# Performance work log

Measured on AMD Instinct MI355X. Metric: run time of the kernel, lower is better.

## Reference

```python
import jax, jax.numpy as jnp
import numpy as np

LAM = 0.5
B, N, C = 512, 197, 384


def _mlp(x, w1, b1, w2, b2):
    # Linear -> exact GELU -> Linear (dropout is identity in eval)
    h = jax.nn.gelu(x @ w1 + b1, approximate=False)
    return h @ w2 + b2


def _ln(x, g, b, eps=1e-5):
    m = jnp.mean(x, axis=-1, keepdims=True)
    v = jnp.mean((x - m) ** 2, axis=-1, keepdims=True)
    return (x - m) * jax.lax.rsqrt(v + eps) * g + b


def _l2norm(x, eps=1e-12):
    n = jnp.sqrt(jnp.sum(x * x, axis=-1, keepdims=True))
    return x / jnp.maximum(n, eps)


def setup_inputs() -> dict:
    key = jax.random.key(0)
    ks = iter(jax.random.split(key, 40))
    s = 0.02

    def w(shape):
        return (jax.random.normal(next(ks), shape, jnp.float32) * s)

    inp = {
        'feat_query': jax.random.normal(next(ks), (B, N, C), jnp.float32),
        'feat_shot': jax.random.normal(next(ks), (B, N, C), jnp.float32),
        'feat_query_start': jax.random.normal(next(ks), (B, N, C), jnp.float32),
        'feat_shot_start': jax.random.normal(next(ks), (B, N, C), jnp.float32),
        # fc1: 384 -> 96 -> 384
        'fc1_w1': w((384, 96)), 'fc1_b1': jnp.zeros((96,)),
        'fc1_w2': w((96, 384)), 'fc1_b2': jnp.zeros((384,)),
        'ln1_g': jnp.ones((384,)), 'ln1_b': jnp.zeros((384,)),
        # fc3: 196 -> 128 -> 196
        'fc3_w1': w((196, 128)), 'fc3_b1': jnp.zeros((128,)),
        'fc3_w2': w((128, 196)), 'fc3_b2': jnp.zeros((196,)),
        'ln3_g': jnp.ones((196,)), 'ln3_b': jnp.zeros((196,)),
        # fc4: 384 -> 96 -> 384
        'fc4_w1': w((384, 96)), 'fc4_b1': jnp.zeros((96,)),
        'fc4_w2': w((96, 384)), 'fc4_b2': jnp.zeros((384,)),
        'ln4_g': jnp.ones((384,)), 'ln4_b': jnp.zeros((384,)),
        # fc2: 9604 -> 256 -> 1
        'fc2_w1': w((98 * 98, 256)), 'fc2_b1': jnp.zeros((256,)),
        'fc2_w2': w((256, 1)), 'fc2_b2': jnp.zeros((1,)),
        # cosine_sim.layer1: 384 -> 96 -> 384
        'cs_w1': w((384, 96)), 'cs_b1': jnp.zeros((96,)),
        'cs_w2': w((96, 384)), 'cs_b2': jnp.zeros((384,)),
    }
    return inp


def reference(feat_query, feat_shot, feat_query_start, feat_shot_start,
              fc1_w1, fc1_b1, fc1_w2, fc1_b2, ln1_g, ln1_b,
              fc3_w1, fc3_b1, fc3_w2, fc3_b2, ln3_g, ln3_b,
              fc4_w1, fc4_b1, fc4_w2, fc4_b2, ln4_g, ln4_b,
              fc2_w1, fc2_b1, fc2_w2, fc2_b2,
              cs_w1, cs_b1, cs_w2, cs_b2):
    def fc1_res(x):  # Mlp over mean token, added back (broadcast over seq)
        m = jnp.mean(x, axis=1, keepdims=True)  # [B,1,C]
        return _ln(_mlp(m, fc1_w1, fc1_b1, fc1_w2, fc1_b2) + x, ln1_g, ln1_b)

    fq = fc1_res(feat_query)
    fs = fc1_res(feat_shot)
    fqs = fc1_res(feat_query_start)
    fss = fc1_res(feat_shot_start)

    query_class = fq[:, 0:1, :]          # [B,1,384]
    query_image = fq[:, 1:, :]           # [B,196,384]
    query_image_start = fqs[:, 1:, :]
    support_class = fs[:, 0:1, :]
    support_image = fs[:, 1:, :]
    support_image_start = fss[:, 1:, :]

    def fc3_path(x):  # Mlp over token dim (196) + LN(196)
        xt = jnp.swapaxes(x, -1, -2)     # [B,384,196]
        xt = _ln(_mlp(xt, fc3_w1, fc3_b1, fc3_w2, fc3_b2), ln3_g, ln3_b)
        return jnp.swapaxes(xt, -1, -2)

    query_image_start = fc3_path(query_image_start)
    support_image_start = fc3_path(support_image_start)

    query_image = _ln(_mlp(query_image * query_image_start, fc4_w1, fc4_b1, fc4_w2, fc4_b2), ln4_g, ln4_b)
    support_image = _ln(_mlp(support_image * support_image_start, fc4_w1, fc4_b1, fc4_w2, fc4_b2), ln4_g, ln4_b)

    fq2 = query_image + LAM * query_class
    fs2 = support_image + LAM * support_class
    fq2 = _l2norm(fq2)
    fq2 = fq2 - jnp.mean(fq2, axis=2, keepdims=True)
    fs2 = _l2norm(fs2)
    fs2 = fs2 - jnp.mean(fs2, axis=2, keepdims=True)

    out = jnp.einsum('bqc,bsc->bqs', fq2, fs2)        # [B,196,196]
    b = out.shape[0]
    out = out.reshape(b, 98, 2, 98, 2).mean(axis=(2, 4))  # AvgPool2d(2,2)
    out = out.reshape(b, 98 * 98)
    out = (_mlp_fc2(out ** 2, fc2_w1, fc2_b1, fc2_w2, fc2_b2)).squeeze(-1)  # [B]

    # Cosine_Sim on class tokens
    qx = _mlp(query_class[:, 0, :], cs_w1, cs_b1, cs_w2, cs_b2)
    sy = _mlp(support_class[:, 0, :], cs_w1, cs_b1, cs_w2, cs_b2)
    eps = 1e-8
    cosine = jnp.sum(qx * sy, axis=-1) / (
        jnp.maximum(jnp.linalg.norm(qx, axis=-1), eps) * jnp.maximum(jnp.linalg.norm(sy, axis=-1), eps))

    return out, cosine, query_class, support_class


def _mlp_fc2(x, w1, b1, w2, b2):
    h = jax.nn.gelu(x @ w1 + b1, approximate=False)
    return h @ w2 + b2
```

## Files before the change

kernel.cpp:

```cpp
#include <hip/hip_runtime.h>
#include <math.h>

typedef unsigned short ushort_t;
typedef __attribute__((ext_vector_type(8))) short bf16x8;
typedef __attribute__((ext_vector_type(4))) float f32x4;

__device__ __forceinline__ float geluf(float x){
  return 0.5f*x*(1.0f+erff(x*0.70710678118654752440f));
}
__device__ __forceinline__ float bfu(unsigned int u){
  union { unsigned int i; float f; } v; v.i = (u & 0xffffu) << 16; return v.f;
}
__device__ __forceinline__ unsigned int f2b(float f){
  union { float f; unsigned int i; } v; v.f = f;
  unsigned int r = v.i + 0x7fffu + ((v.i >> 16) & 1u);
  return (r >> 16);
}


__global__ __launch_bounds__(384) void k_mean(
    const float* __restrict__ x0, const float* __restrict__ x1,
    const float* __restrict__ x2, const float* __restrict__ x3,
    float* __restrict__ meanb){
  __shared__ float4 red[4][96];
  int sb = blockIdx.x;
  int s = sb >> 9, b = sb & 511;
  const float* x = (s==0)?x0:(s==1)?x1:(s==2)?x2:x3;
  int tid = threadIdx.x;
  int c4 = tid % 96, g = tid / 96;
  const float* p = x + ((size_t)b*197)*384 + c4*4;
  float4 acc = {0.f,0.f,0.f,0.f};
  for (int t = g; t < 197; t += 4){
    float4 v = *reinterpret_cast<const float4*>(p + (size_t)t*384);
    acc.x += v.x; acc.y += v.y; acc.z += v.z; acc.w += v.w;
  }
  red[g][c4] = acc;
  __syncthreads();
  if (tid < 96){
    float4 a = red[0][tid], bb = red[1][tid], c = red[2][tid], d = red[3][tid];
    float4 o;
    o.x = (a.x+bb.x+c.x+d.x)*(1.0f/197.0f);
    o.y = (a.y+bb.y+c.y+d.y)*(1.0f/197.0f);
    o.z = (a.z+bb.z+c.z+d.z)*(1.0f/197.0f);
    o.w = (a.w+bb.w+c.w+d.w)*(1.0f/197.0f);
    *reinterpret_cast<float4*>(&meanb[(size_t)sb*384 + tid*4]) = o;
  }
}

__global__ __launch_bounds__(384) void k_fc1(
    const float* __restrict__ meanb, const float* __restrict__ w1,
    const float* __restrict__ b1, const float* __restrict__ w2,
    const float* __restrict__ b2, float* __restrict__ mlp1){
  __shared__ float ms[384];
  __shared__ float hs[96];
  int row = blockIdx.x, tid = threadIdx.x;
  ms[tid] = meanb[(size_t)row*384 + tid];
  __syncthreads();
  if (tid < 96){
    float a = b1[tid];
    for (int c=0;c<384;++c) a += ms[c]*w1[c*96+tid];
    hs[tid] = geluf(a);
  }
  __syncthreads();
  float a = b2[tid];
  for (int j=0;j<96;++j) a += hs[j]*w2[j*384+tid];
  mlp1[(size_t)row*384 + tid] = a;
}

__global__ __launch_bounds__(256) void k_stats(
    const float* __restrict__ x0, const float* __restrict__ x1,
    const float* __restrict__ x2, const float* __restrict__ x3,
    const float* __restrict__ mlp1, float* __restrict__ mu, float* __restrict__ rstd){
  int sb = blockIdx.x;
  int s = sb >> 9, b = sb & 511;
  const float* x = (s==0)?x0:(s==1)?x1:(s==2)?x2:x3;
  const float* mp = mlp1 + (size_t)sb*384;
  int tid = threadIdx.x, w = tid >> 6, lane = tid & 63;
  int g = lane >> 4, il = lane & 15;
  float4 mreg[6];
  #pragma unroll
  for (int it = 0; it < 6; ++it)
    mreg[it] = *reinterpret_cast<const float4*>(&mp[il*4 + 64*it]);
  for (int t0 = 0; t0 < 208; t0 += 16){
    int t = t0 + w*4 + g;
    if (t < 197){
      const float* xp = x + ((size_t)b*197 + t)*384 + il*4;
      float sum = 0.f, sq = 0.f;
      #pragma unroll
      for (int it = 0; it < 6; ++it){
        float4 v = *reinterpret_cast<const float4*>(xp + 64*it);
        float a0 = v.x + mreg[it].x, a1 = v.y + mreg[it].y;
        float a2 = v.z + mreg[it].z, a3 = v.w + mreg[it].w;
        sum += a0+a1+a2+a3;
        sq  += a0*a0+a1*a1+a2*a2+a3*a3;
      }
      #pragma unroll
      for (int o=1;o<16;o<<=1){ sum += __shfl_xor(sum,o); sq += __shfl_xor(sq,o); }
      if (il == 0){
        int row = sb*197 + t;
        float m = sum*(1.0f/384.0f);
        mu[row] = m;
        rstd[row] = rsqrtf(sq*(1.0f/384.0f) - m*m + 1e-5f);
      }
    }
  }
}

__global__ __launch_bounds__(384) void k_class(
    const float* __restrict__ x0, const float* __restrict__ x1,
    const float* __restrict__ mlp1, const float* __restrict__ mu,
    const float* __restrict__ rstd, const float* __restrict__ g1,
    const float* __restrict__ bb1, float* __restrict__ dout){
  int s = blockIdx.x >> 9, b = blockIdx.x & 511, c = threadIdx.x;
  const float* x = s ? x1 : x0;
  int srow = (s*512 + b)*197;
  float v = x[((size_t)b*197)*384 + c] + mlp1[((size_t)s*512+b)*384 + c];
  float y = (v - mu[srow])*rstd[srow]*g1[c] + bb1[c];
  dout[1024 + (size_t)s*196608 + (size_t)b*384 + c] = y;
}

__global__ __launch_bounds__(384) void k_cosine(
    const float* __restrict__ w1, const float* __restrict__ b1,
    const float* __restrict__ w2, const float* __restrict__ b2,
    float* __restrict__ dout){
  __shared__ float qrow[384], srw[384], hq[96], hs[96];
  __shared__ float rd0[384], rd1[384], rd2[384];
  int b = blockIdx.x, tid = threadIdx.x;
  qrow[tid] = dout[1024   + (size_t)b*384 + tid];
  srw[tid]  = dout[197632 + (size_t)b*384 + tid];
  __syncthreads();
  if (tid < 96){
    float a = b1[tid];
    for (int c=0;c<384;++c) a += qrow[c]*w1[c*96+tid];
    hq[tid] = geluf(a);
  } else if (tid < 192){
    int j = tid - 96;
    float a = b1[j];
    for (int c=0;c<384;++c) a += srw[c]*w1[c*96+j];
    hs[j] = geluf(a);
  }
  __syncthreads();
  float qx = b2[tid], sy = b2[tid];
  for (int j=0;j<96;++j){ qx += hq[j]*w2[j*384+tid]; sy += hs[j]*w2[j*384+tid]; }
  rd0[tid] = qx*sy; rd1[tid] = qx*qx; rd2[tid] = sy*sy;
  __syncthreads();
  if (tid < 64){
    float d=0.f,nq=0.f,ns=0.f;
    for (int i=tid;i<384;i+=64){ d+=rd0[i]; nq+=rd1[i]; ns+=rd2[i]; }
    #pragma unroll
    for (int o=32;o;o>>=1){ d+=__shfl_down(d,o); nq+=__shfl_down(nq,o); ns+=__shfl_down(ns,o); }
    if (tid==0) dout[512 + b] = d / (fmaxf(sqrtf(nq),1e-8f)*fmaxf(sqrtf(ns),1e-8f));
  }
}

__global__ __launch_bounds__(256) void k_wt(
    const float* __restrict__ w1_4, const float* __restrict__ w2_4,
    const float* __restrict__ w1_3, const float* __restrict__ w2_3,
    ushort_t* __restrict__ w1t, ushort_t* __restrict__ w2t,
    ushort_t* __restrict__ w1t3, ushort_t* __restrict__ w2t3){
  int idx = blockIdx.x*256 + threadIdx.x;
  if (idx < 36864){
    int c = idx / 96, j = idx - c*96;
    w2t[idx] = (ushort_t)f2b(w2_4[(size_t)j*384 + c]);
  } else if (idx < 73728){
    int k = idx - 36864;
    int j = k / 384, c = k - j*384;
    w1t[k] = (ushort_t)f2b(w1_4[(size_t)c*96 + j]);
  } else if (idx < 102400){
    int k = idx - 73728;
    int j = k / 224, t = k - j*224;
    w1t3[k] = (t < 196) ? (ushort_t)f2b(w1_3[(size_t)t*128 + j]) : (ushort_t)0;
  } else {
    int k = idx - 102400;
    int tp = k / 128, j = k - tp*128;
    w2t3[k] = (tp < 196) ? (ushort_t)f2b(w2_3[(size_t)j*196 + tp]) : (ushort_t)0;
  }
}

__global__ __launch_bounds__(256) void k_fc3(
    const float* __restrict__ x,
    const float* __restrict__ m1_base,
    const float* __restrict__ mu_s,
    const float* __restrict__ rstd_s,
    const float* __restrict__ g1, const float* __restrict__ bln1,
    const ushort_t* __restrict__ w1t3,
    const float* __restrict__ b1,
    const ushort_t* __restrict__ w2t3,
    const float* __restrict__ b2, const float* __restrict__ g3,
    const float* __restrict__ b3,
    ushort_t* __restrict__ Qout){
  __shared__ ushort_t Xs[64][232];
  __shared__ ushort_t W2s[112][136];
  __shared__ float m1s[64], g1s[64], b1s[64];
  __shared__ float mus[196], rss[196];
  __shared__ float b1j[128];
  __shared__ float b2s[208], g3s[208], b3s[208];
  int bid = blockIdx.x;
  int b = bid/6, c0 = (bid%6)*64;
  int tid = threadIdx.x;
  if (tid < 64){
    m1s[tid] = m1_base[(size_t)b*384 + c0 + tid];
    g1s[tid] = g1[c0+tid]; b1s[tid] = bln1[c0+tid];
  }
  if (tid < 128) b1j[tid] = b1[tid];
  if (tid < 196){ mus[tid] = mu_s[b*197 + tid + 1]; rss[tid] = rstd_s[b*197 + tid + 1]; }
  if (tid < 208){
    float bb=0.f, gg=0.f, b3v=0.f;
    if (tid < 196){ bb = b2[tid]; gg = g3[tid]; b3v = b3[tid]; }
    b2s[tid]=bb; g3s[tid]=gg; b3s[tid]=b3v;
  }
  for (int i = tid; i < 112*16; i += 256){
    int r = i >> 4, q = i & 15;
    *reinterpret_cast<uint4*>(&W2s[r][q*8]) =
        *reinterpret_cast<const uint4*>(&w2t3[(size_t)r*128 + q*8]);
  }
  for (int i = tid; i < 64*14; i += 256){
    *reinterpret_cast<unsigned int*>(&Xs[i/14][196 + 2*(i%14)]) = 0u;
  }
  __syncthreads();
  for (int e = 0; e < 7; ++e){
    int idx = e*256 + tid;
    if (idx < 1568){
      int t2 = idx >> 4, c4 = idx & 15;
      int t0 = t2*2;
      const float* xr = &x[((size_t)b*197 + t0 + 1)*384 + c0 + c4*4];
      float4 xv0 = *reinterpret_cast<const float4*>(xr);
      float4 xv1 = *reinterpret_cast<const float4*>(xr + 384);
      float mu0 = mus[t0], rs0 = rss[t0], mu1 = mus[t0+1], rs1 = rss[t0+1];
      int c = c4*4;
      unsigned int u0 = f2b(((xv0.x + m1s[c+0]) - mu0)*rs0*g1s[c+0] + b1s[c+0])
                      | (f2b(((xv1.x + m1s[c+0]) - mu1)*rs1*g1s[c+0] + b1s[c+0]) << 16);
      unsigned int u1 = f2b(((xv0.y + m1s[c+1]) - mu0)*rs0*g1s[c+1] + b1s[c+1])
                      | (f2b(((xv1.y + m1s[c+1]) - mu1)*rs1*g1s[c+1] + b1s[c+1]) << 16);
      unsigned int u2 = f2b(((xv0.z + m1s[c+2]) - mu0)*rs0*g1s[c+2] + b1s[c+2])
                      | (f2b(((xv1.z + m1s[c+2]) - mu1)*rs1*g1s[c+2] + b1s[c+2]) << 16);
      unsigned int u3 = f2b(((xv0.w + m1s[c+3]) - mu0)*rs0*g1s[c+3] + b1s[c+3])
                      | (f2b(((xv1.w + m1s[c+3]) - mu1)*rs1*g1s[c+3] + b1s[c+3]) << 16);
      *reinterpret_cast<unsigned int*>(&Xs[c+0][t0]) = u0;
      *reinterpret_cast<unsigned int*>(&Xs[c+1][t0]) = u1;
      *reinterpret_cast<unsigned int*>(&Xs[c+2][t0]) = u2;
      *reinterpret_cast<unsigned int*>(&Xs[c+3][t0]) = u3;
    }
  }
  __syncthreads();
  int w = tid >> 6, lane = tid & 63;
  int cl = lane & 15, kg = lane >> 4;
  f32x4 hacc[8];
  #pragma unroll
  for (int jf=0;jf<8;++jf){ f32x4 z={0.f,0.f,0.f,0.f}; hacc[jf]=z; }
  const ushort_t* zrow = &Xs[w*16 + cl][kg*8];
  const ushort_t* abase = w1t3 + (size_t)cl*224 + kg*8;
  bf16x8 aC[8], aN[8];
  #pragma unroll
  for (int jf=0;jf<8;++jf)
    aC[jf] = *reinterpret_cast<const bf16x8*>(abase + jf*16*224);
  for (int kc = 0; kc < 7; ++kc){
    bf16x8 xb = *reinterpret_cast<const bf16x8*>(zrow + kc*32);
    if (kc < 6){
      #pragma unroll
      for (int jf=0;jf<8;++jf)
        aN[jf] = *reinterpret_cast<const bf16x8*>(abase + jf*16*224 + (kc+1)*32);
    }
    #pragma unroll
    for (int jf=0;jf<8;++jf)
      hacc[jf] = __builtin_amdgcn_mfma_f32_16x16x32_bf16(aC[jf], xb, hacc[jf], 0, 0, 0);
    #pragma unroll
    for (int jf=0;jf<8;++jf) aC[jf] = aN[jf];
  }
  #pragma unroll
  for (int jf=0;jf<8;++jf){
    f32x4 y = hacc[jf];
    int j0 = jf*16 + kg*4;
    uint2 pk;
    pk.x = f2b(geluf(y[0]+b1j[j0+0])) | (f2b(geluf(y[1]+b1j[j0+1]))<<16);
    pk.y = f2b(geluf(y[2]+b1j[j0+2])) | (f2b(geluf(y[3]+b1j[j0+3]))<<16);
    *reinterpret_cast<uint2*>(&Xs[w*16 + cl][j0]) = pk;
  }
  f32x4 yacc[13];
  #pragma unroll
  for (int tf=0;tf<13;++tf){ f32x4 z={0.f,0.f,0.f,0.f}; yacc[tf]=z; }
  const ushort_t* hrow = &Xs[w*16 + cl][kg*8];
  for (int kc = 0; kc < 4; ++kc){
    bf16x8 hb = *reinterpret_cast<const bf16x8*>(hrow + kc*32);
    #pragma unroll
    for (int tf=0;tf<7;++tf){
      const ushort_t* bp = &W2s[tf*16 + cl][kg*8 + kc*32];
      yacc[tf] = __builtin_amdgcn_mfma_f32_16x16x32_bf16(
          hb, *reinterpret_cast<const bf16x8*>(bp), yacc[tf], 0, 0, 0);
    }
  }
  __syncthreads();
  for (int i = tid; i < 96*16; i += 256){
    int r = i >> 4, q = i & 15;
    *reinterpret_cast<uint4*>(&W2s[r][q*8]) =
        *reinterpret_cast<const uint4*>(&w2t3[(size_t)(112 + r)*128 + q*8]);
  }
  __syncthreads();
  for (int kc = 0; kc < 4; ++kc){
    bf16x8 hb = *reinterpret_cast<const bf16x8*>(hrow + kc*32);
    #pragma unroll
    for (int tf=7;tf<13;++tf){
      const ushort_t* bp = &W2s[tf*16 + cl - 112][kg*8 + kc*32];
      yacc[tf] = __builtin_amdgcn_mfma_f32_16x16x32_bf16(
          hb, *reinterpret_cast<const bf16x8*>(bp), yacc[tf], 0, 0, 0);
    }
  }
  float sum0=0.f,sum1=0.f,sum2=0.f,sum3=0.f, sq0=0.f,sq1=0.f,sq2=0.f,sq3=0.f;
  #pragma unroll
  for (int tf=0;tf<13;++tf){
    int tp = tf*16 + cl;
    float bb = b2s[tp];
    f32x4 y = yacc[tf];
    y[0]+=bb; y[1]+=bb; y[2]+=bb; y[3]+=bb;
    yacc[tf] = y;
    sum0+=y[0]; sum1+=y[1]; sum2+=y[2]; sum3+=y[3];
    sq0+=y[0]*y[0]; sq1+=y[1]*y[1]; sq2+=y[2]*y[2]; sq3+=y[3]*y[3];
  }
  #pragma unroll
  for (int o=1;o<16;o<<=1){
    sum0+=__shfl_xor(sum0,o); sum1+=__shfl_xor(sum1,o);
    sum2+=__shfl_xor(sum2,o); sum3+=__shfl_xor(sum3,o);
    sq0+=__shfl_xor(sq0,o); sq1+=__shfl_xor(sq1,o);
    sq2+=__shfl_xor(sq2,o); sq3+=__shfl_xor(sq3,o);
  }
  float m0=sum0*(1.0f/196.0f), m1v=sum1*(1.0f/196.0f), m2=sum2*(1.0f/196.0f), m3=sum3*(1.0f/196.0f);
  float r0=rsqrtf(sq0*(1.0f/196.0f)-m0*m0+1e-5f);
  float r1=rsqrtf(sq1*(1.0f/196.0f)-m1v*m1v+1e-5f);
  float r2=rsqrtf(sq2*(1.0f/196.0f)-m2*m2+1e-5f);
  float r3=rsqrtf(sq3*(1.0f/196.0f)-m3*m3+1e-5f);
  int cbase = c0 + w*16 + kg*4;
  #pragma unroll
  for (int tf=0;tf<13;++tf){
    int tp = tf*16 + cl;
    if (tp < 196){
      float gg = g3s[tp], bb3 = b3s[tp];
      f32x4 y = yacc[tf];
      unsigned int o0 = f2b((y[0]-m0)*r0*gg + bb3);
      unsigned int o1 = f2b((y[1]-m1v)*r1*gg + bb3);
      unsigned int o2 = f2b((y[2]-m2)*r2*gg + bb3);
      unsigned int o3 = f2b((y[3]-m3)*r3*gg + bb3);
      uint2 pk; pk.x = o0 | (o1<<16); pk.y = o2 | (o3<<16);
      *reinterpret_cast<uint2*>(&Qout[((size_t)b*196 + tp)*384 + cbase]) = pk;
    }
  }
}

__global__ __launch_bounds__(256) void k_fc4a(
    const float* __restrict__ x,
    const float* __restrict__ m1_base,
    const float* __restrict__ mu_s,
    const float* __restrict__ rstd_s,
    const float* __restrict__ g1, const float* __restrict__ bln1,
    const ushort_t* __restrict__ Qin,
    const ushort_t* __restrict__ w1t,
    const float* __restrict__ b1mlp,
    ushort_t* __restrict__ h4s){
  __shared__ ushort_t Zs[64][392];
  __shared__ float m1s[384], g1s[384], b1s[384];
  __shared__ float mus[64], rss[64];
  __shared__ float b1m[96];
  int bid = blockIdx.x;
  int b = bid >> 2, tt0 = (bid & 3)*64;
  int tid = threadIdx.x;
  const float* m1 = m1_base + (size_t)b*384;
  for (int i = tid; i < 384; i += 256){ m1s[i] = m1[i]; g1s[i] = g1[i]; b1s[i] = bln1[i]; }
  if (tid < 96) b1m[tid] = b1mlp[tid];
  if (tid < 64){
    int t = tt0 + tid; int tc = t < 196 ? t : 195;
    mus[tid] = mu_s[b*197 + tc + 1]; rss[tid] = rstd_s[b*197 + tc + 1];
  }
  __syncthreads();
  for (int e = 0; e < 24; ++e){
    int v = e*256 + tid;
    int row = v/96, col4 = v - row*96;
    int t = tt0 + row; int tc = t < 196 ? t : 195;
    float valid = (t < 196) ? 1.f : 0.f;
    float4 xv = *reinterpret_cast<const float4*>(&x[((size_t)b*197 + tc + 1)*384 + col4*4]);
    uint2 qv = *reinterpret_cast<const uint2*>(&Qin[((size_t)b*196 + tc)*384 + col4*4]);
    float muv = mus[row], rsv = rss[row];
    int c = col4*4;
    float z0 = (((xv.x + m1s[c+0]) - muv)*rsv*g1s[c+0] + b1s[c+0]) * bfu(qv.x)      * valid;
    float z1 = (((xv.y + m1s[c+1]) - muv)*rsv*g1s[c+1] + b1s[c+1]) * bfu(qv.x>>16)  * valid;
    float z2 = (((xv.z + m1s[c+2]) - muv)*rsv*g1s[c+2] + b1s[c+2]) * bfu(qv.y)      * valid;
    float z3 = (((xv.w + m1s[c+3]) - muv)*rsv*g1s[c+3] + b1s[c+3]) * bfu(qv.y>>16)  * valid;
    uint2 pk; pk.x = f2b(z0) | (f2b(z1)<<16); pk.y = f2b(z2) | (f2b(z3)<<16);
    *reinterpret_cast<uint2*>(&Zs[row][col4*4]) = pk;
  }
  __syncthreads();
  int w = tid >> 6, lane = tid & 63;
  int tr = tt0 + w*16 + (lane & 15);
  int kg = lane >> 4;
  f32x4 acc0 = {0.f,0.f,0.f,0.f}, acc1 = {0.f,0.f,0.f,0.f}, acc2 = {0.f,0.f,0.f,0.f};
  f32x4 acc3 = {0.f,0.f,0.f,0.f}, acc4 = {0.f,0.f,0.f,0.f}, acc5 = {0.f,0.f,0.f,0.f};
  const ushort_t* arow = w1t + (size_t)(lane & 15)*384 + kg*8;
  const ushort_t* zrow = &Zs[w*16 + (lane & 15)][kg*8];
  for (int kc = 0; kc < 12; ++kc){
    bf16x8 zb = *reinterpret_cast<const bf16x8*>(zrow + kc*32);
    bf16x8 a0 = *reinterpret_cast<const bf16x8*>(arow + kc*32);
    bf16x8 a1 = *reinterpret_cast<const bf16x8*>(arow + kc*32 + 16*384);
    bf16x8 a2 = *reinterpret_cast<const bf16x8*>(arow + kc*32 + 32*384);
    bf16x8 a3 = *reinterpret_cast<const bf16x8*>(arow + kc*32 + 48*384);
    bf16x8 a4 = *reinterpret_cast<const bf16x8*>(arow + kc*32 + 64*384);
    bf16x8 a5 = *reinterpret_cast<const bf16x8*>(arow + kc*32 + 80*384);
    acc0 = __builtin_amdgcn_mfma_f32_16x16x32_bf16(a0, zb, acc0, 0, 0, 0);
    acc1 = __builtin_amdgcn_mfma_f32_16x16x32_bf16(a1, zb, acc1, 0, 0, 0);
    acc2 = __builtin_amdgcn_mfma_f32_16x16x32_bf16(a2, zb, acc2, 0, 0, 0);
    acc3 = __builtin_amdgcn_mfma_f32_16x16x32_bf16(a3, zb, acc3, 0, 0, 0);
    acc4 = __builtin_amdgcn_mfma_f32_16x16x32_bf16(a4, zb, acc4, 0, 0, 0);
    acc5 = __builtin_amdgcn_mfma_f32_16x16x32_bf16(a5, zb, acc5, 0, 0, 0);
  }
  if (tr < 196){
    ushort_t* dst = h4s + ((size_t)b*196 + tr)*96 + kg*4;
    #pragma unroll
    for (int jb = 0; jb < 6; ++jb){
      f32x4 y = (jb==0)?acc0:(jb==1)?acc1:(jb==2)?acc2:(jb==3)?acc3:(jb==4)?acc4:acc5;
      int j0 = jb*16 + kg*4;
      uint2 pk;
      pk.x = f2b(geluf(y[0]+b1m[j0+0])) | (f2b(geluf(y[1]+b1m[j0+1]))<<16);
      pk.y = f2b(geluf(y[2]+b1m[j0+2])) | (f2b(geluf(y[3]+b1m[j0+3]))<<16);
      *reinterpret_cast<uint2*>(dst + jb*16) = pk;
    }
  }
}

__global__ __launch_bounds__(256) void k_fc4b(
    const ushort_t* __restrict__ h4s,
    const ushort_t* __restrict__ w2t,
    const float* __restrict__ b2, const float* __restrict__ g4,
    const float* __restrict__ bb4,
    const float* __restrict__ cls_base,
    ushort_t* __restrict__ Qo){
  __shared__ float b2s[384], g4s[384], b4s[384], cl_s[384];
  int bid = blockIdx.x;
  int b = bid >> 2, ttile = bid & 3;
  int tid = threadIdx.x, w = tid >> 6, lane = tid & 63;
  const float* cls = cls_base + (size_t)b*384;
  for (int i = tid; i < 384; i += 256){
    b2s[i] = b2[i]; g4s[i] = g4[i]; b4s[i] = bb4[i]; cl_s[i] = cls[i];
  }
  __syncthreads();
  int tr = ttile*64 + w*16 + (lane & 15);
  int trc = tr < 196 ? tr : 195;
  int kg = lane >> 4;
  const ushort_t* hp = h4s + ((size_t)b*196 + trc)*96 + kg*8;
  bf16x8 hb0 = *reinterpret_cast<const bf16x8*>(hp);
  bf16x8 hb1 = *reinterpret_cast<const bf16x8*>(hp + 32);
  bf16x8 hb2 = *reinterpret_cast<const bf16x8*>(hp + 64);
  const ushort_t* ap_base = w2t + (size_t)(lane & 15)*96 + kg*8;
  f32x4 acc[24];
  #pragma unroll
  for (int af = 0; af < 24; ++af){
    const ushort_t* ap = ap_base + (size_t)af*16*96;
    bf16x8 a0 = *reinterpret_cast<const bf16x8*>(ap);
    bf16x8 a1 = *reinterpret_cast<const bf16x8*>(ap + 32);
    bf16x8 a2 = *reinterpret_cast<const bf16x8*>(ap + 64);
    f32x4 z = {0.f,0.f,0.f,0.f};
    z = __builtin_amdgcn_mfma_f32_16x16x32_bf16(a0, hb0, z, 0, 0, 0);
    z = __builtin_amdgcn_mfma_f32_16x16x32_bf16(a1, hb1, z, 0, 0, 0);
    z = __builtin_amdgcn_mfma_f32_16x16x32_bf16(a2, hb2, z, 0, 0, 0);
    acc[af] = z;
  }
  float sum = 0.f, sq = 0.f;
  #pragma unroll
  for (int af = 0; af < 24; ++af){
    int cb = af*16 + kg*4;
    float4 bv = *reinterpret_cast<const float4*>(&b2s[cb]);
    f32x4 y = acc[af];
    y[0] += bv.x; y[1] += bv.y; y[2] += bv.z; y[3] += bv.w;
    acc[af] = y;
    sum += y[0]+y[1]+y[2]+y[3];
    sq  += y[0]*y[0]+y[1]*y[1]+y[2]*y[2]+y[3]*y[3];
  }
  sum += __shfl_xor(sum, 16); sum += __shfl_xor(sum, 32);
  sq  += __shfl_xor(sq, 16);  sq  += __shfl_xor(sq, 32);
  float m4 = sum*(1.0f/384.0f);
  float rs = rsqrtf(sq*(1.0f/384.0f) - m4*m4 + 1e-5f);
  float s2 = 0.f;
  #pragma unroll
  for (int af = 0; af < 24; ++af){
    int cb = af*16 + kg*4;
    float4 gv = *reinterpret_cast<const float4*>(&g4s[cb]);
    float4 bb = *reinterpret_cast<const float4*>(&b4s[cb]);
    float4 cv = *reinterpret_cast<const float4*>(&cl_s[cb]);
    f32x4 y = acc[af];
    y[0] = (y[0]-m4)*rs*gv.x + bb.x + 0.5f*cv.x;
    y[1] = (y[1]-m4)*rs*gv.y + bb.y + 0.5f*cv.y;
    y[2] = (y[2]-m4)*rs*gv.z + bb.z + 0.5f*cv.z;
    y[3] = (y[3]-m4)*rs*gv.w + bb.w + 0.5f*cv.w;
    acc[af] = y;
    s2 += y[0]*y[0]+y[1]*y[1]+y[2]*y[2]+y[3]*y[3];
  }
  s2 += __shfl_xor(s2, 16); s2 += __shfl_xor(s2, 32);
  float inv = 1.0f/fmaxf(sqrtf(s2), 1e-12f);
  float sm = 0.f;
  #pragma unroll
  for (int af = 0; af < 24; ++af){
    f32x4 y = acc[af];
    y[0]*=inv; y[1]*=inv; y[2]*=inv; y[3]*=inv;
    acc[af] = y;
    sm += y[0]+y[1]+y[2]+y[3];
  }
  sm += __shfl_xor(sm, 16); sm += __shfl_xor(sm, 32);
  sm *= (1.0f/384.0f);
  if (tr < 196){
    ushort_t* dst = Qo + ((size_t)b*196 + tr)*384 + kg*4;
    #pragma unroll
    for (int af = 0; af < 24; ++af){
      f32x4 y = acc[af];
      uint2 pk;
      pk.x = f2b(y[0]-sm) | (f2b(y[1]-sm)<<16);
      pk.y = f2b(y[2]-sm) | (f2b(y[3]-sm)<<16);
      *reinterpret_cast<uint2*>(dst + af*16) = pk;
    }
  }
}

__global__ __launch_bounds__(256) void k_sim(
    const ushort_t* __restrict__ Q, const ushort_t* __restrict__ S,
    float* __restrict__ P){
  int bid0 = blockIdx.x;
  int bx = (bid0 & 7)*1024 + (bid0 >> 3);
  int b = bx >> 4, qt = (bx >> 2) & 3, st = bx & 3;
  int tid = threadIdx.x;
  int w = tid >> 6, lane = tid & 63;
  int wr = w >> 1, wc = w & 1;
  int q0 = qt*64 + wr*32, s0 = st*64 + wc*32;
  int rrow = lane & 15, kg = lane >> 4;
  const ushort_t* Qb_ = Q + (size_t)b*196*384;
  const ushort_t* Sb_ = S + (size_t)b*196*384;
  int qr0 = min(q0 + rrow, 195), qr1 = min(q0 + 16 + rrow, 195);
  int sr0 = min(s0 + rrow, 195), sr1 = min(s0 + 16 + rrow, 195);
  const ushort_t* qp0 = Qb_ + (size_t)qr0*384 + kg*8;
  const ushort_t* qp1 = Qb_ + (size_t)qr1*384 + kg*8;
  const ushort_t* sp0 = Sb_ + (size_t)sr0*384 + kg*8;
  const ushort_t* sp1 = Sb_ + (size_t)sr1*384 + kg*8;
  f32x4 acc00 = {0.f,0.f,0.f,0.f}, acc01 = {0.f,0.f,0.f,0.f};
  f32x4 acc10 = {0.f,0.f,0.f,0.f}, acc11 = {0.f,0.f,0.f,0.f};
  bf16x8 qa0 = *reinterpret_cast<const bf16x8*>(qp0);
  bf16x8 qa1 = *reinterpret_cast<const bf16x8*>(qp1);
  bf16x8 sa0 = *reinterpret_cast<const bf16x8*>(sp0);
  bf16x8 sa1 = *reinterpret_cast<const bf16x8*>(sp1);
  for (int kc = 0; kc < 11; ++kc){
    int koff = (kc+1)*32;
    bf16x8 nq0 = *reinterpret_cast<const bf16x8*>(qp0 + koff);
    bf16x8 nq1 = *reinterpret_cast<const bf16x8*>(qp1 + koff);
    bf16x8 ns0 = *reinterpret_cast<const bf16x8*>(sp0 + koff);
    bf16x8 ns1 = *reinterpret_cast<const bf16x8*>(sp1 + koff);
    acc00 = __builtin_amdgcn_mfma_f32_16x16x32_bf16(qa0, sa0, acc00, 0, 0, 0);
    acc01 = __builtin_amdgcn_mfma_f32_16x16x32_bf16(qa0, sa1, acc01, 0, 0, 0);
    acc10 = __builtin_amdgcn_mfma_f32_16x16x32_bf16(qa1, sa0, acc10, 0, 0, 0);
    acc11 = __builtin_amdgcn_mfma_f32_16x16x32_bf16(qa1, sa1, acc11, 0, 0, 0);
    qa0 = nq0; qa1 = nq1; sa0 = ns0; sa1 = ns1;
  }
  acc00 = __builtin_amdgcn_mfma_f32_16x16x32_bf16(qa0, sa0, acc00, 0, 0, 0);
  acc01 = __builtin_amdgcn_mfma_f32_16x16x32_bf16(qa0, sa1, acc01, 0, 0, 0);
  acc10 = __builtin_amdgcn_mfma_f32_16x16x32_bf16(qa1, sa0, acc10, 0, 0, 0);
  acc11 = __builtin_amdgcn_mfma_f32_16x16x32_bf16(qa1, sa1, acc11, 0, 0, 0);
  int c = lane & 15, g = lane >> 4;
  float* Pb = P + (size_t)b*98*98;
  #pragma unroll
  for (int i = 0; i < 2; ++i){
    #pragma unroll
    for (int j = 0; j < 2; ++j){
      f32x4 v = (i==0) ? (j==0 ? acc00 : acc01) : (j==0 ? acc10 : acc11);
      float p0 = v[0] + v[1];
      float p1 = v[2] + v[3];
      float t0 = p0 + __shfl_xor(p0, 1);
      float t1 = p1 + __shfl_xor(p1, 1);
      if (!(c & 1)){
        int qp = (q0 + 16*i + 4*g) >> 1;
        int sp = (s0 + 16*j + c) >> 1;
        if (sp < 98){
          if (qp     < 98) Pb[(size_t)(qp    )*98 + sp] = 0.25f*t0;
          if (qp + 1 < 98) Pb[(size_t)(qp + 1)*98 + sp] = 0.25f*t1;
        }
      }
    }
  }
}

__global__ __launch_bounds__(256) void k_fc2a(
    const float* __restrict__ P, const float* __restrict__ w1,
    float* __restrict__ Cpart){
  __shared__ float p2[8][688];
  int bx = blockIdx.x;
  int mb = bx & 63, ks = bx >> 6;
  int b0 = mb*8, k0 = ks*686;
  int tid = threadIdx.x;
  for (int idx = tid; idx < 8*686; idx += 256){
    int r = idx / 686, i = idx - r*686;
    float v = P[(size_t)(b0+r)*9604 + k0 + i];
    p2[r][i] = v*v;
  }
  __syncthreads();
  float acc[8];
  #pragma unroll
  for (int r=0;r<8;++r) acc[r]=0.f;
  for (int ii=0; ii<686; ++ii){
    float w = w1[(size_t)(k0+ii)*256 + tid];
    #pragma unroll
    for (int r=0;r<8;++r) acc[r] += p2[r][ii]*w;
  }
  #pragma unroll
  for (int r=0;r<8;++r) Cpart[((size_t)ks*512 + b0 + r)*256 + tid] = acc[r];
}

__global__ __launch_bounds__(256) void k_fc2b(
    const float* __restrict__ Cpart, const float* __restrict__ b1,
    const float* __restrict__ w2, const float* __restrict__ b2,
    float* __restrict__ outp){
  __shared__ float red[4];
  int b = blockIdx.x, tid = threadIdx.x;
  float s = 0.f;
  for (int ks = 0; ks < 14; ++ks) s += Cpart[((size_t)ks*512 + b)*256 + tid];
  float h = geluf(s + b1[tid]) * w2[tid];
  #pragma unroll
  for (int o=32;o;o>>=1) h += __shfl_down(h,o);
  int w = tid >> 6, lane = tid & 63;
  if (lane==0) red[w] = h;
  __syncthreads();
  if (tid==0) outp[b] = red[0]+red[1]+red[2]+red[3] + b2[0];
}

extern "C" void kernel_launch(void* const* d_in, const int* in_sizes, int n_in,
                              void* d_out, int out_size, void* d_ws, size_t ws_size,
                              hipStream_t stream){
  const float* fq  = (const float*)d_in[0];
  const float* fs  = (const float*)d_in[1];
  const float* fqs = (const float*)d_in[2];
  const float* fss = (const float*)d_in[3];
  const float* fc1_w1 = (const float*)d_in[4];
  const float* fc1_b1 = (const float*)d_in[5];
  const float* fc1_w2 = (const float*)d_in[6];
  const float* fc1_b2 = (const float*)d_in[7];
  const float* ln1_g = (const float*)d_in[8];
  const float* ln1_b = (const float*)d_in[9];
  const float* fc3_w1 = (const float*)d_in[10];
  const float* fc3_b1 = (const float*)d_in[11];
  const float* fc3_w2 = (const float*)d_in[12];
  const float* fc3_b2 = (const float*)d_in[13];
  const float* ln3_g = (const float*)d_in[14];
  const float* ln3_b = (const float*)d_in[15];
  const float* fc4_w1 = (const float*)d_in[16];
  const float* fc4_b1 = (const float*)d_in[17];
  const float* fc4_w2 = (const float*)d_in[18];
  const float* fc4_b2 = (const float*)d_in[19];
  const float* ln4_g = (const float*)d_in[20];
  const float* ln4_b = (const float*)d_in[21];
  const float* fc2_w1 = (const float*)d_in[22];
  const float* fc2_b1 = (const float*)d_in[23];
  const float* fc2_w2 = (const float*)d_in[24];
  const float* fc2_b2 = (const float*)d_in[25];
  const float* cs_w1 = (const float*)d_in[26];
  const float* cs_b1 = (const float*)d_in[27];
  const float* cs_w2 = (const float*)d_in[28];
  const float* cs_b2 = (const float*)d_in[29];
  float* out = (float*)d_out;
  char* ws = (char*)d_ws;
  float* meanb  = (float*)(ws + 0);
  ushort_t* w2t  = (ushort_t*)(ws + 0);
  ushort_t* w1t  = (ushort_t*)(ws + 73728);
  ushort_t* w1t3 = (ushort_t*)(ws + 147456);
  ushort_t* w2t3 = (ushort_t*)(ws + 204800);
  float* mlp1   = (float*)(ws + 3145728);
  float* mu     = (float*)(ws + 6291456);
  float* rstd   = (float*)(ws + 7905280);
  ushort_t* h4  = (ushort_t*)(ws + 9519104);
  float* P      = (float*)(ws + 9519104);
  float* Cpart  = (float*)(ws + 29188096);
  ushort_t* Qb  = (ushort_t*)(ws + 59850752);
  ushort_t* Sb  = (ushort_t*)(ws + 136921088);
  const size_t H4S = (size_t)512*196*96;

  k_mean<<<2048, 384, 0, stream>>>(fq, fs, fqs, fss, meanb);
  k_fc1<<<2048, 384, 0, stream>>>(meanb, fc1_w1, fc1_b1, fc1_w2, fc1_b2, mlp1);
  k_wt<<<504, 256, 0, stream>>>(fc4_w1, fc4_w2, fc3_w1, fc3_w2,
                                w1t, w2t, w1t3, w2t3);
  k_stats<<<2048, 256, 0, stream>>>(fq, fs, fqs, fss, mlp1, mu, rstd);
  k_class<<<1024, 384, 0, stream>>>(fq, fs, mlp1, mu, rstd, ln1_g, ln1_b, out);
  k_cosine<<<512, 384, 0, stream>>>(cs_w1, cs_b1, cs_w2, cs_b2, out);
  k_fc3<<<3072, 256, 0, stream>>>(fqs, mlp1 + (size_t)2*512*384, mu + 2*100864, rstd + 2*100864,
                                  ln1_g, ln1_b, w1t3, fc3_b1, w2t3, fc3_b2, ln3_g, ln3_b, Qb);
  k_fc3<<<3072, 256, 0, stream>>>(fss, mlp1 + (size_t)3*512*384, mu + 3*100864, rstd + 3*100864,
                                  ln1_g, ln1_b, w1t3, fc3_b1, w2t3, fc3_b2, ln3_g, ln3_b, Sb);
  k_fc4a<<<2048, 256, 0, stream>>>(fq, mlp1, mu, rstd, ln1_g, ln1_b,
                                   Qb, w1t, fc4_b1, h4);
  k_fc4a<<<2048, 256, 0, stream>>>(fs, mlp1 + (size_t)512*384, mu + 100864, rstd + 100864,
                                   ln1_g, ln1_b, Sb, w1t, fc4_b1, h4 + H4S);
  k_fc4b<<<2048, 256, 0, stream>>>(h4,       w2t, fc4_b2, ln4_g, ln4_b, out + 1024,          Qb);
  k_fc4b<<<2048, 256, 0, stream>>>(h4 + H4S, w2t, fc4_b2, ln4_g, ln4_b, out + 1024 + 196608, Sb);
  k_sim<<<8192, 256, 0, stream>>>(Qb, Sb, P);
  k_fc2a<<<896, 256, 0, stream>>>(P, fc2_w1, Cpart);
  k_fc2b<<<512, 256, 0, stream>>>(Cpart, fc2_b1, fc2_w2, fc2_b2, out);
}
```

Before: 1.372 ms.

## Fuse token mean, fc1 MLP and LayerNorm stats into one kernel via LDS cache

Merges the mean, fc1 and stats kernels into one per-(stream,batch) kernel. The input tile is cached in LDS as bf16 during the mean pass, so the LayerNorm statistics are computed without a second global read of the four large inputs. This removes two launches and one full input pass. The cost is about 151KB of LDS per block, which limits occupancy to one block per CU, and the statistics now come from bf16-rounded values, which reduces their accuracy.

```diff
diff --git a/kernel.cpp b/kernel.cpp
--- a/kernel.cpp
+++ b/kernel.cpp
@@ -18,86 +18,85 @@
 }
 
 
-__global__ __launch_bounds__(384) void k_mean(
+__global__ __launch_bounds__(384) void k_ms(
     const float* __restrict__ x0, const float* __restrict__ x1,
     const float* __restrict__ x2, const float* __restrict__ x3,
-    float* __restrict__ meanb){
+    const float* __restrict__ w1, const float* __restrict__ b1,
+    const float* __restrict__ w2, const float* __restrict__ b2,
+    float* __restrict__ mlp1, float* __restrict__ mu, float* __restrict__ rstd){
+  __shared__ ushort_t Xb[197][384];
   __shared__ float4 red[4][96];
+  __shared__ float ms[384];
+  __shared__ float hs[96];
+  __shared__ float m1s[384];
   int sb = blockIdx.x;
   int s = sb >> 9, b = sb & 511;
   const float* x = (s==0)?x0:(s==1)?x1:(s==2)?x2:x3;
   int tid = threadIdx.x;
   int c4 = tid % 96, g = tid / 96;
   const float* p = x + ((size_t)b*197)*384 + c4*4;
-  float4 acc = {0.f,0.f,0.f,0.f};
-  for (int t = g; t < 197; t += 4){
+  float4 a0 = {0.f,0.f,0.f,0.f}, a1 = {0.f,0.f,0.f,0.f};
+  int t = g;
+  for (; t + 4 < 197; t += 8){
+    float4 v0 = *reinterpret_cast<const float4*>(p + (size_t)t*384);
+    float4 v1 = *reinterpret_cast<const float4*>(p + (size_t)(t+4)*384);
+    uint2 pk0; pk0.x = f2b(v0.x) | (f2b(v0.y)<<16); pk0.y = f2b(v0.z) | (f2b(v0.w)<<16);
+    uint2 pk1; pk1.x = f2b(v1.x) | (f2b(v1.y)<<16); pk1.y = f2b(v1.z) | (f2b(v1.w)<<16);
+    *reinterpret_cast<uint2*>(&Xb[t][c4*4]) = pk0;
+    *reinterpret_cast<uint2*>(&Xb[t+4][c4*4]) = pk1;
+    a0.x += v0.x; a0.y += v0.y; a0.z += v0.z; a0.w += v0.w;
+    a1.x += v1.x; a1.y += v1.y; a1.z += v1.z; a1.w += v1.w;
+  }
+  if (t < 197){
     float4 v = *reinterpret_cast<const float4*>(p + (size_t)t*384);
-    acc.x += v.x; acc.y += v.y; acc.z += v.z; acc.w += v.w;
-  }
-  red[g][c4] = acc;
+    uint2 pk; pk.x = f2b(v.x) | (f2b(v.y)<<16); pk.y = f2b(v.z) | (f2b(v.w)<<16);
+    *reinterpret_cast<uint2*>(&Xb[t][c4*4]) = pk;
+    a0.x += v.x; a0.y += v.y; a0.z += v.z; a0.w += v.w;
+  }
+  a0.x += a1.x; a0.y += a1.y; a0.z += a1.z; a0.w += a1.w;
+  red[g][c4] = a0;
   __syncthreads();
   if (tid < 96){
     float4 a = red[0][tid], bb = red[1][tid], c = red[2][tid], d = red[3][tid];
-    float4 o;
-    o.x = (a.x+bb.x+c.x+d.x)*(1.0f/197.0f);
-    o.y = (a.y+bb.y+c.y+d.y)*(1.0f/197.0f);
-    o.z = (a.z+bb.z+c.z+d.z)*(1.0f/197.0f);
-    o.w = (a.w+bb.w+c.w+d.w)*(1.0f/197.0f);
-    *reinterpret_cast<float4*>(&meanb[(size_t)sb*384 + tid*4]) = o;
-  }
-}
-
-__global__ __launch_bounds__(384) void k_fc1(
-    const float* __restrict__ meanb, const float* __restrict__ w1,
-    const float* __restrict__ b1, const float* __restrict__ w2,
-    const float* __restrict__ b2, float* __restrict__ mlp1){
-  __shared__ float ms[384];
-  __shared__ float hs[96];
-  int row = blockIdx.x, tid = threadIdx.x;
-  ms[tid] = meanb[(size_t)row*384 + tid];
+    ms[tid*4+0] = (a.x+bb.x+c.x+d.x)*(1.0f/197.0f);
+    ms[tid*4+1] = (a.y+bb.y+c.y+d.y)*(1.0f/197.0f);
+    ms[tid*4+2] = (a.z+bb.z+c.z+d.z)*(1.0f/197.0f);
+    ms[tid*4+3] = (a.w+bb.w+c.w+d.w)*(1.0f/197.0f);
+  }
   __syncthreads();
   if (tid < 96){
     float a = b1[tid];
-    for (int c=0;c<384;++c) a += ms[c]*w1[c*96+tid];
+    for (int c = 0; c < 384; ++c) a += ms[c]*w1[c*96+tid];
     hs[tid] = geluf(a);
   }
   __syncthreads();
-  float a = b2[tid];
-  for (int j=0;j<96;++j) a += hs[j]*w2[j*384+tid];
-  mlp1[(size_t)row*384 + tid] = a;
-}
-
-__global__ __launch_bounds__(256) void k_stats(
-    const float* __restrict__ x0, const float* __restrict__ x1,
-    const float* __restrict__ x2, const float* __restrict__ x3,
-    const float* __restrict__ mlp1, float* __restrict__ mu, float* __restrict__ rstd){
-  int sb = blockIdx.x;
-  int s = sb >> 9, b = sb & 511;
-  const float* x = (s==0)?x0:(s==1)?x1:(s==2)?x2:x3;
-  const float* mp = mlp1 + (size_t)sb*384;
-  int tid = threadIdx.x, w = tid >> 6, lane = tid & 63;
-  int g = lane >> 4, il = lane & 15;
-  float4 mreg[6];
-  #pragma unroll
-  for (int it = 0; it < 6; ++it)
-    mreg[it] = *reinterpret_cast<const float4*>(&mp[il*4 + 64*it]);
-  for (int t0 = 0; t0 < 208; t0 += 16){
-    int t = t0 + w*4 + g;
-    if (t < 197){
-      const float* xp = x + ((size_t)b*197 + t)*384 + il*4;
+  {
+    float a = b2[tid];
+    for (int j = 0; j < 96; ++j) a += hs[j]*w2[j*384+tid];
+    m1s[tid] = a;
+    mlp1[(size_t)sb*384 + tid] = a;
+  }
+  __syncthreads();
+  int grp = tid >> 4, il = tid & 15;
+  for (int it = 0; it < 9; ++it){
+    int tr = it*24 + grp;
+    if (tr < 197){
       float sum = 0.f, sq = 0.f;
       #pragma unroll
-      for (int it = 0; it < 6; ++it){
-        float4 v = *reinterpret_cast<const float4*>(xp + 64*it);
-        float a0 = v.x + mreg[it].x, a1 = v.y + mreg[it].y;
-        float a2 = v.z + mreg[it].z, a3 = v.w + mreg[it].w;
-        sum += a0+a1+a2+a3;
-        sq  += a0*a0+a1*a1+a2*a2+a3*a3;
+      for (int e = 0; e < 6; ++e){
+        int c = il*4 + e*64;
+        uint2 v = *reinterpret_cast<const uint2*>(&Xb[tr][c]);
+        float q0 = bfu(v.x)      + m1s[c+0];
+        float q1 = bfu(v.x>>16)  + m1s[c+1];
+        float q2 = bfu(v.y)      + m1s[c+2];
+        float q3 = bfu(v.y>>16)  + m1s[c+3];
+        sum += q0+q1+q2+q3;
+        sq  += q0*q0+q1*q1+q2*q2+q3*q3;
       }
       #pragma unroll
       for (int o=1;o<16;o<<=1){ sum += __shfl_xor(sum,o); sq += __shfl_xor(sq,o); }
       if (il == 0){
-        int row = sb*197 + t;
+        int row = sb*197 + tr;
         float m = sum*(1.0f/384.0f);
         mu[row] = m;
         rstd[row] = rsqrtf(sq*(1.0f/384.0f) - m*m + 1e-5f);
@@ -657,7 +656,6 @@
   const float* cs_b2 = (const float*)d_in[29];
   float* out = (float*)d_out;
   char* ws = (char*)d_ws;
-  float* meanb  = (float*)(ws + 0);
   ushort_t* w2t  = (ushort_t*)(ws + 0);
   ushort_t* w1t  = (ushort_t*)(ws + 73728);
   ushort_t* w1t3 = (ushort_t*)(ws + 147456);
@@ -672,11 +670,11 @@
   ushort_t* Sb  = (ushort_t*)(ws + 136921088);
   const size_t H4S = (size_t)512*196*96;
 
-  k_mean<<<2048, 384, 0, stream>>>(fq, fs, fqs, fss, meanb);
-  k_fc1<<<2048, 384, 0, stream>>>(meanb, fc1_w1, fc1_b1, fc1_w2, fc1_b2, mlp1);
   k_wt<<<504, 256, 0, stream>>>(fc4_w1, fc4_w2, fc3_w1, fc3_w2,
                                 w1t, w2t, w1t3, w2t3);
-  k_stats<<<2048, 256, 0, stream>>>(fq, fs, fqs, fss, mlp1, mu, rstd);
+  k_ms<<<2048, 384, 0, stream>>>(fq, fs, fqs, fss,
+                                 fc1_w1, fc1_b1, fc1_w2, fc1_b2,
+                                 mlp1, mu, rstd);
   k_class<<<1024, 384, 0, stream>>>(fq, fs, mlp1, mu, rstd, ln1_g, ln1_b, out);
   k_cosine<<<512, 384, 0, stream>>>(cs_w1, cs_b1, cs_w2, cs_b2, out);
   k_fc3<<<3072, 256, 0, stream>>>(fqs, mlp1 + (size_t)2*512*384, mu + 2*100864, rstd + 2*100864,
```

New measurement: 1.378 ms. Within noise of the previous version (+0.4%).
